# Kernel tuning notes

Measured on AMD Instinct MI355X. Metric: run time of the kernel, lower is better.

The kernel has to match this reference:

```python
import jax, jax.numpy as jnp
import numpy as np
from jax import lax

BN_EPS = 1e-5

@jax.custom_vjp
def ste_sign(x):
    # Binarize to {-1, +1} (sign; 0 maps to 0 like torch.sign, negligible measure)
    return jnp.sign(x)

def _ste_fwd(x):
    return jnp.sign(x), x

def _ste_bwd(x, g):
    # Straight-through estimator: pass gradient where |x| <= 1
    return (g * (jnp.abs(x) <= 1.0).astype(g.dtype),)

ste_sign.defvjp(_ste_fwd, _ste_bwd)

def bin_conv3x3(x, w, stride=1):
    # Binarize both activations and weights, then 3x3 conv, padding=1, no bias
    xb = ste_sign(x)
    wb = ste_sign(w)
    return lax.conv_general_dilated(
        xb, wb, window_strides=(stride, stride), padding=((1, 1), (1, 1)),
        dimension_numbers=('NCHW', 'OIHW', 'NCHW'))

def batchnorm_inf(x, gamma, beta, mean, var):
    # Inference-mode BatchNorm2d over channel dim (axis=1)
    scale = gamma * lax.rsqrt(var + BN_EPS)
    shift = beta - mean * scale
    return x * scale[None, :, None, None] + shift[None, :, None, None]

def hardtanh(x):
    # SelfTanh modeled as hardtanh (standard BNN activation with STE-style grad)
    return jnp.clip(x, -1.0, 1.0)

def setup_inputs() -> dict:
    key = jax.random.key(0)
    ks = jax.random.split(key, 3)
    N, C, H, W = 64, 256, 56, 56
    x = jax.random.normal(ks[0], (N, C, H, W), dtype=jnp.float32)
    w1 = jax.random.normal(ks[1], (C, C, 3, 3), dtype=jnp.float32) * (1.0 / math_sqrt(9 * C))
    w2 = jax.random.normal(ks[2], (C, C, 3, 3), dtype=jnp.float32) * (1.0 / math_sqrt(9 * C))
    ones = jnp.ones((C,), jnp.float32)
    zeros = jnp.zeros((C,), jnp.float32)
    return {
        'x': x,
        'w1': w1, 'g1': ones, 'b1': zeros, 'm1': zeros, 'v1': ones,
        'w2': w2, 'g2': ones, 'b2': zeros, 'm2': zeros, 'v2': ones,
    }

def math_sqrt(v):
    return float(np.sqrt(v))

def reference(x, w1, g1, b1, m1, v1, w2, g2, b2, m2, v2):
    residual = x
    out = bin_conv3x3(x, w1, stride=1)
    out = batchnorm_inf(out, g1, b1, m1, v1)
    out = hardtanh(out)
    out = bin_conv3x3(out, w2, stride=1)
    out = batchnorm_inf(out, g2, b2, m2, v2)
    out = out + residual
    out = hardtanh(out)
    return out
```

## Files before the change

### kernel.cpp

```cpp
#include <hip/hip_runtime.h>
#include <stdint.h>


#define NB 64
#define C  256
#define H  56
#define W  56
#define HP 58
#define PPIX 272
#define SLOT (HP * PPIX)
#define OST 272

typedef int v4i __attribute__((ext_vector_type(4)));

__global__ __launch_bounds__(256)
void pack_x_kernel(const float* __restrict__ x, int8_t* __restrict__ Aq) {
    const int h = blockIdx.x, n = blockIdx.y;
    const int w  = threadIdx.x & 63;
    const int cq = threadIdx.x >> 6;

    __shared__ int8_t st[56 * OST];

    const float* xp = x + (((size_t)n * C + cq * 64) * H + h) * W + w;
#pragma unroll
    for (int i = 0; i < 16; ++i) {
        uint32_t u = 0;
#pragma unroll
        for (int b = 0; b < 4; ++b) {
            float v = (w < 56) ? xp[(size_t)(i * 4 + b) * (H * W)] : 0.0f;
            uint32_t t = (v < 0.0f) ? 0xFFu : ((v != 0.0f) ? 1u : 0u);
            u |= t << (8 * b);
        }
        if (w < 56)
            *(uint32_t*)(st + w * OST + cq * 64 + i * 4) = u;
    }
    __syncthreads();
    int8_t* dst = Aq + (((size_t)n * HP + h + 1) * HP + 1) * C;
    for (int idx = threadIdx.x; idx < 56 * 16; idx += 256) {
        int pix = idx >> 4, c16 = idx & 15;
        *(v4i*)(dst + (size_t)pix * C + c16 * 16) =
            *(const v4i*)(st + pix * OST + c16 * 16);
    }
}

__global__ __launch_bounds__(64)
void pack_w_kernel(const float* __restrict__ wa, const float* __restrict__ wb,
                   int8_t* __restrict__ B1, int8_t* __restrict__ B2) {
    const int kstep = blockIdx.x;
    const int nfrag = blockIdx.y;
    const float* wsrc = blockIdx.z ? wb : wa;
    int8_t* dst       = blockIdx.z ? B2 : B1;
    const int lane = threadIdx.x, quad = lane >> 4, l16 = lane & 15;
    const int co = nfrag * 16 + l16;
    uint32_t pk[4];
#pragma unroll
    for (int d = 0; d < 4; ++d) {
        uint32_t u = 0;
#pragma unroll
        for (int bb = 0; bb < 4; ++bb) {
            int k = kstep * 64 + quad * 16 + d * 4 + bb;
            int tap = k >> 8, ci = k & 255;
            float v = wsrc[((size_t)co * C + ci) * 9 + tap];
            uint32_t t = (v < 0.0f) ? 0xFFu : ((v != 0.0f) ? 1u : 0u);
            u |= t << (8 * bb);
        }
        pk[d] = u;
    }
    uint4 st; st.x = pk[0]; st.y = pk[1]; st.z = pk[2]; st.w = pk[3];
    *(uint4*)(dst + ((size_t)(nfrag * 36 + kstep) * 64 + lane) * 16) = st;
}

__global__ __launch_bounds__(256)
void halo_zero_kernel(int8_t* __restrict__ Aq, int8_t* __restrict__ Bq) {
    const int n = blockIdx.x;
    int8_t* buf = blockIdx.y ? Bq : Aq;
    const v4i z = (v4i){0, 0, 0, 0};
    for (int idx = threadIdx.x; idx < 228 * 16; idx += 256) {
        int px = idx >> 4, c16 = idx & 15;
        int row, col;
        if (px < 58)       { row = 0;  col = px; }
        else if (px < 116) { row = 57; col = px - 58; }
        else { int i = px - 116; row = 1 + (i >> 1); col = (i & 1) * 57; }
        *(v4i*)(buf + (((size_t)n * HP + row) * HP + col) * C + c16 * 16) = z;
    }
}

__global__ __launch_bounds__(256)
void bn_prep_kernel(const float* g1, const float* b1, const float* m1, const float* v1,
                    const float* g2, const float* b2, const float* m2, const float* v2,
                    float* __restrict__ sc, float* __restrict__ sh) {
    const int co = threadIdx.x;
    const float* g = blockIdx.x ? g2 : g1;
    const float* b = blockIdx.x ? b2 : b1;
    const float* m = blockIdx.x ? m2 : m1;
    const float* v = blockIdx.x ? v2 : v1;
    double scd = (double)g[co] / sqrt((double)v[co] + 1e-5);
    sc[blockIdx.x * C + co] = (float)scd;
    sh[blockIdx.x * C + co] = (float)((double)b[co] - (double)m[co] * scd);
}

template <int STAGE>
__global__ __launch_bounds__(512, 4)
void mconv_kernel(const int8_t* __restrict__ Aq, const int8_t* __restrict__ Bpk,
                  const float* __restrict__ scp, const float* __restrict__ shp,
                  const float* __restrict__ resid,
                  int8_t* __restrict__ Bout, float* __restrict__ out) {
    const int h2 = blockIdx.x;
    const int n  = blockIdx.y;
    const int tid = threadIdx.x;
    const int wv = tid >> 6, lane = tid & 63, quad = lane >> 4, l16 = lane & 15;

    __shared__ int8_t lds[4 * SLOT];

    const int8_t* gA = Aq + ((size_t)n * HP + h2 * 2) * HP * C;
    for (int idx = tid; idx < 4 * HP * 16; idx += 512) {
        int pix = idx >> 4, c16 = idx & 15;
        *(v4i*)(lds + pix * PPIX + c16 * 16) =
            *(const v4i*)(gA + (size_t)pix * C + c16 * 16);
    }
    __syncthreads();

    int abase[7];
#pragma unroll
    for (int f = 0; f < 7; ++f) {
        int mm = f * 16 + l16;
        int hl = (mm >= 56) ? 1 : 0;
        int w  = mm - 56 * hl;
        abase[f] = hl * SLOT + w * PPIX + quad * 16;
    }

    const int8_t* bq[2];
#pragma unroll
    for (int nf = 0; nf < 2; ++nf)
        bq[nf] = Bpk + (size_t)((wv * 2 + nf) * 36) * 1024 + lane * 16;

    v4i bcur[2];
#pragma unroll
    for (int nf = 0; nf < 2; ++nf) bcur[nf] = *(const v4i*)(bq[nf]);

    v4i acc[7][2];
#pragma unroll
    for (int f = 0; f < 7; ++f)
#pragma unroll
        for (int nf = 0; nf < 2; ++nf) acc[f][nf] = (v4i){0, 0, 0, 0};

#pragma unroll 1
    for (int t = 0; t < 9; ++t) {
        const int r = (t >= 6) ? 2 : ((t >= 3) ? 1 : 0);
        const int c = t - 3 * r;
        const int au = r * SLOT + c * PPIX;
#pragma unroll
        for (int ci = 0; ci < 4; ++ci) {
            v4i bnxt[2];
#pragma unroll
            for (int nf = 0; nf < 2; ++nf)
                bnxt[nf] = *(const v4i*)(bq[nf] + (ci + 1) * 1024);
            v4i afr[7];
#pragma unroll
            for (int f = 0; f < 7; ++f)
                afr[f] = *(const v4i*)(lds + abase[f] + au + ci * 64);
            __builtin_amdgcn_s_setprio(1);
#pragma unroll
            for (int f = 0; f < 7; ++f)
#pragma unroll
                for (int nf = 0; nf < 2; ++nf)
                    acc[f][nf] = __builtin_amdgcn_mfma_i32_16x16x64_i8(
                        afr[f], bcur[nf], acc[f][nf], 0, 0, 0);
            __builtin_amdgcn_s_setprio(0);
#pragma unroll
            for (int nf = 0; nf < 2; ++nf) bcur[nf] = bnxt[nf];
        }
#pragma unroll
        for (int nf = 0; nf < 2; ++nf) bq[nf] += 4096;
    }

    if (STAGE == 1) {
        __syncthreads();
#pragma unroll
        for (int nf = 0; nf < 2; ++nf) {
            const int co = (wv * 2 + nf) * 16 + l16;
            const float scale = scp[co], shift = shp[co];
#pragma unroll
            for (int f = 0; f < 7; ++f) {
#pragma unroll
                for (int reg = 0; reg < 4; ++reg) {
                    int mm = f * 16 + quad * 4 + reg;
                    float v = __fadd_rn(__fmul_rn((float)acc[f][nf][reg], scale), shift);
                    int8_t t8 = (v < 0.0f) ? (int8_t)-1
                              : ((v != 0.0f) ? (int8_t)1 : (int8_t)0);
                    lds[mm * OST + co] = t8;
                }
            }
        }
        __syncthreads();
        for (int idx = tid; idx < 112 * 16; idx += 512) {
            int mm = idx >> 4, c16 = idx & 15;
            int hl = (mm >= 56) ? 1 : 0;
            int ww = mm - 56 * hl;
            int oh = h2 * 2 + hl;
            *(v4i*)(Bout + (((size_t)n * HP + oh + 1) * HP + ww + 1) * C + c16 * 16)
                = *(const v4i*)(lds + mm * OST + c16 * 16);
        }
    } else {
#pragma unroll
        for (int nf = 0; nf < 2; ++nf) {
            const int co = (wv * 2 + nf) * 16 + l16;
            const float scale = scp[co], shift = shp[co];
#pragma unroll
            for (int f = 0; f < 7; ++f) {
                int mmb = f * 16 + quad * 4;
                int hl = (mmb >= 56) ? 1 : 0;
                int w0 = mmb - 56 * hl;
                int oh = h2 * 2 + hl;
                size_t ridx = (((size_t)n * C + co) * H + oh) * W + w0;
                float4 rv = *(const float4*)(resid + ridx);
                float rr[4] = {rv.x, rv.y, rv.z, rv.w};
                float oo[4];
#pragma unroll
                for (int reg = 0; reg < 4; ++reg) {
                    float v = __fadd_rn(__fmul_rn((float)acc[f][nf][reg], scale), shift);
                    float o = v + rr[reg];
                    oo[reg] = fminf(1.0f, fmaxf(-1.0f, o));
                }
                float4 ov; ov.x = oo[0]; ov.y = oo[1]; ov.z = oo[2]; ov.w = oo[3];
                *(float4*)(out + ridx) = ov;
            }
        }
    }
}

extern "C" void kernel_launch(void* const* d_in, const int* in_sizes, int n_in,
                              void* d_out, int out_size, void* d_ws, size_t ws_size,
                              hipStream_t stream) {
    const float* x  = (const float*)d_in[0];
    const float* w1 = (const float*)d_in[1];
    const float* g1 = (const float*)d_in[2];
    const float* b1 = (const float*)d_in[3];
    const float* m1 = (const float*)d_in[4];
    const float* v1 = (const float*)d_in[5];
    const float* w2 = (const float*)d_in[6];
    const float* g2 = (const float*)d_in[7];
    const float* b2 = (const float*)d_in[8];
    const float* m2 = (const float*)d_in[9];
    const float* v2 = (const float*)d_in[10];
    float* out = (float*)d_out;

    uint8_t* ws = (uint8_t*)d_ws;
    const size_t ASZ = (size_t)NB * HP * HP * C;
    const size_t WPK = (size_t)16 * 36 * 64 * 16;
    int8_t* Aq   = (int8_t*)(ws);
    int8_t* Bq   = (int8_t*)(ws + ASZ);
    int8_t* Bpk1 = (int8_t*)(ws + 2 * ASZ);
    int8_t* Bpk2 = (int8_t*)(ws + 2 * ASZ + WPK);
    float*  scb  = (float*)(ws + 2 * ASZ + 2 * WPK);
    float*  shb  = (float*)(ws + 2 * ASZ + 2 * WPK + 2048);

    halo_zero_kernel<<<dim3(NB, 2), 256, 0, stream>>>(Aq, Bq);
    bn_prep_kernel<<<dim3(2), 256, 0, stream>>>(g1, b1, m1, v1, g2, b2, m2, v2,
                                                scb, shb);
    pack_w_kernel<<<dim3(36, 16, 2), 64, 0, stream>>>(w1, w2, Bpk1, Bpk2);
    pack_x_kernel<<<dim3(H, NB), 256, 0, stream>>>(x, Aq);
    mconv_kernel<1><<<dim3(28, NB), 512, 0, stream>>>(Aq, Bpk1, scb, shb,
                                                      nullptr, Bq, nullptr);
    mconv_kernel<2><<<dim3(28, NB), 512, 0, stream>>>(Bq, Bpk2, scb + C, shb + C,
                                                      x, nullptr, out);
}
```

Before: 605.6 us.

## Process one output row per block instead of two, raising occupancy

```diff
diff --git a/kernel.cpp b/kernel.cpp
--- a/kernel.cpp
+++ b/kernel.cpp
@@ -100,47 +100,37 @@
 }
 
 template <int STAGE>
-__global__ __launch_bounds__(512, 4)
+__global__ __launch_bounds__(512, 6)
 void mconv_kernel(const int8_t* __restrict__ Aq, const int8_t* __restrict__ Bpk,
                   const float* __restrict__ scp, const float* __restrict__ shp,
                   const float* __restrict__ resid,
                   int8_t* __restrict__ Bout, float* __restrict__ out) {
-    const int h2 = blockIdx.x;
+    const int oh = blockIdx.x;
     const int n  = blockIdx.y;
     const int tid = threadIdx.x;
     const int wv = tid >> 6, lane = tid & 63, quad = lane >> 4, l16 = lane & 15;
 
-    __shared__ int8_t lds[4 * SLOT];
-
-    const int8_t* gA = Aq + ((size_t)n * HP + h2 * 2) * HP * C;
-    for (int idx = tid; idx < 4 * HP * 16; idx += 512) {
+    __shared__ int8_t lds[3 * SLOT + 8 * PPIX];
+
+    const int8_t* gA = Aq + ((size_t)n * HP + oh) * HP * C;
+    for (int idx = tid; idx < 3 * HP * 16; idx += 512) {
         int pix = idx >> 4, c16 = idx & 15;
         *(v4i*)(lds + pix * PPIX + c16 * 16) =
             *(const v4i*)(gA + (size_t)pix * C + c16 * 16);
     }
     __syncthreads();
 
-    int abase[7];
-#pragma unroll
-    for (int f = 0; f < 7; ++f) {
-        int mm = f * 16 + l16;
-        int hl = (mm >= 56) ? 1 : 0;
-        int w  = mm - 56 * hl;
-        abase[f] = hl * SLOT + w * PPIX + quad * 16;
-    }
-
-    const int8_t* bq[2];
-#pragma unroll
-    for (int nf = 0; nf < 2; ++nf)
-        bq[nf] = Bpk + (size_t)((wv * 2 + nf) * 36) * 1024 + lane * 16;
-
-    v4i bcur[2];
-#pragma unroll
-    for (int nf = 0; nf < 2; ++nf) bcur[nf] = *(const v4i*)(bq[nf]);
-
-    v4i acc[7][2];
-#pragma unroll
-    for (int f = 0; f < 7; ++f)
+    int abase[4];
+#pragma unroll
+    for (int f = 0; f < 4; ++f)
+        abase[f] = (f * 16 + l16) * PPIX + quad * 16;
+
+    const int8_t* bq0 = Bpk + (size_t)((wv * 2 + 0) * 36) * 1024 + lane * 16;
+    const int8_t* bq1 = Bpk + (size_t)((wv * 2 + 1) * 36) * 1024 + lane * 16;
+
+    v4i acc[4][2];
+#pragma unroll
+    for (int f = 0; f < 4; ++f)
 #pragma unroll
         for (int nf = 0; nf < 2; ++nf) acc[f][nf] = (v4i){0, 0, 0, 0};
 
@@ -151,27 +141,24 @@
         const int au = r * SLOT + c * PPIX;
 #pragma unroll
         for (int ci = 0; ci < 4; ++ci) {
-            v4i bnxt[2];
-#pragma unroll
-            for (int nf = 0; nf < 2; ++nf)
-                bnxt[nf] = *(const v4i*)(bq[nf] + (ci + 1) * 1024);
-            v4i afr[7];
-#pragma unroll
-            for (int f = 0; f < 7; ++f)
+            v4i b0 = *(const v4i*)(bq0 + ci * 1024);
+            v4i b1 = *(const v4i*)(bq1 + ci * 1024);
+            v4i afr[4];
+#pragma unroll
+            for (int f = 0; f < 4; ++f)
                 afr[f] = *(const v4i*)(lds + abase[f] + au + ci * 64);
             __builtin_amdgcn_s_setprio(1);
 #pragma unroll
-            for (int f = 0; f < 7; ++f)
-#pragma unroll
-                for (int nf = 0; nf < 2; ++nf)
-                    acc[f][nf] = __builtin_amdgcn_mfma_i32_16x16x64_i8(
-                        afr[f], bcur[nf], acc[f][nf], 0, 0, 0);
+            for (int f = 0; f < 4; ++f) {
+                acc[f][0] = __builtin_amdgcn_mfma_i32_16x16x64_i8(
+                    afr[f], b0, acc[f][0], 0, 0, 0);
+                acc[f][1] = __builtin_amdgcn_mfma_i32_16x16x64_i8(
+                    afr[f], b1, acc[f][1], 0, 0, 0);
+            }
             __builtin_amdgcn_s_setprio(0);
-#pragma unroll
-            for (int nf = 0; nf < 2; ++nf) bcur[nf] = bnxt[nf];
-        }
-#pragma unroll
-        for (int nf = 0; nf < 2; ++nf) bq[nf] += 4096;
+        }
+        bq0 += 4096;
+        bq1 += 4096;
     }
 
     if (STAGE == 1) {
@@ -181,25 +168,24 @@
             const int co = (wv * 2 + nf) * 16 + l16;
             const float scale = scp[co], shift = shp[co];
 #pragma unroll
-            for (int f = 0; f < 7; ++f) {
+            for (int f = 0; f < 4; ++f) {
 #pragma unroll
                 for (int reg = 0; reg < 4; ++reg) {
                     int mm = f * 16 + quad * 4 + reg;
-                    float v = __fadd_rn(__fmul_rn((float)acc[f][nf][reg], scale), shift);
-                    int8_t t8 = (v < 0.0f) ? (int8_t)-1
-                              : ((v != 0.0f) ? (int8_t)1 : (int8_t)0);
-                    lds[mm * OST + co] = t8;
+                    if (mm < 56) {
+                        float v = __fadd_rn(__fmul_rn((float)acc[f][nf][reg], scale), shift);
+                        int8_t t8 = (v < 0.0f) ? (int8_t)-1
+                                  : ((v != 0.0f) ? (int8_t)1 : (int8_t)0);
+                        lds[mm * OST + co] = t8;
+                    }
                 }
             }
         }
         __syncthreads();
-        for (int idx = tid; idx < 112 * 16; idx += 512) {
-            int mm = idx >> 4, c16 = idx & 15;
-            int hl = (mm >= 56) ? 1 : 0;
-            int ww = mm - 56 * hl;
-            int oh = h2 * 2 + hl;
+        for (int idx = tid; idx < 56 * 16; idx += 512) {
+            int ww = idx >> 4, c16 = idx & 15;
             *(v4i*)(Bout + (((size_t)n * HP + oh + 1) * HP + ww + 1) * C + c16 * 16)
-                = *(const v4i*)(lds + mm * OST + c16 * 16);
+                = *(const v4i*)(lds + ww * OST + c16 * 16);
         }
     } else {
 #pragma unroll
@@ -207,23 +193,22 @@
             const int co = (wv * 2 + nf) * 16 + l16;
             const float scale = scp[co], shift = shp[co];
 #pragma unroll
-            for (int f = 0; f < 7; ++f) {
+            for (int f = 0; f < 4; ++f) {
                 int mmb = f * 16 + quad * 4;
-                int hl = (mmb >= 56) ? 1 : 0;
-                int w0 = mmb - 56 * hl;
-                int oh = h2 * 2 + hl;
-                size_t ridx = (((size_t)n * C + co) * H + oh) * W + w0;
-                float4 rv = *(const float4*)(resid + ridx);
-                float rr[4] = {rv.x, rv.y, rv.z, rv.w};
-                float oo[4];
-#pragma unroll
-                for (int reg = 0; reg < 4; ++reg) {
-                    float v = __fadd_rn(__fmul_rn((float)acc[f][nf][reg], scale), shift);
-                    float o = v + rr[reg];
-                    oo[reg] = fminf(1.0f, fmaxf(-1.0f, o));
+                if (mmb < 56) {
+                    size_t ridx = (((size_t)n * C + co) * H + oh) * W + mmb;
+                    float4 rv = *(const float4*)(resid + ridx);
+                    float rr[4] = {rv.x, rv.y, rv.z, rv.w};
+                    float oo[4];
+#pragma unroll
+                    for (int reg = 0; reg < 4; ++reg) {
+                        float v = __fadd_rn(__fmul_rn((float)acc[f][nf][reg], scale), shift);
+                        float o = v + rr[reg];
+                        oo[reg] = fminf(1.0f, fmaxf(-1.0f, o));
+                    }
+                    float4 ov; ov.x = oo[0]; ov.y = oo[1]; ov.z = oo[2]; ov.w = oo[3];
+                    *(float4*)(out + ridx) = ov;
                 }
-                float4 ov; ov.x = oo[0]; ov.y = oo[1]; ov.z = oo[2]; ov.w = oo[3];
-                *(float4*)(out + ridx) = ov;
             }
         }
     }
@@ -260,8 +245,8 @@
                                                 scb, shb);
     pack_w_kernel<<<dim3(36, 16, 2), 64, 0, stream>>>(w1, w2, Bpk1, Bpk2);
     pack_x_kernel<<<dim3(H, NB), 256, 0, stream>>>(x, Aq);
-    mconv_kernel<1><<<dim3(28, NB), 512, 0, stream>>>(Aq, Bpk1, scb, shb,
-                                                      nullptr, Bq, nullptr);
-    mconv_kernel<2><<<dim3(28, NB), 512, 0, stream>>>(Bq, Bpk2, scb + C, shb + C,
-                                                      x, nullptr, out);
-}
+    mconv_kernel<1><<<dim3(H, NB), 512, 0, stream>>>(Aq, Bpk1, scb, shb,
+                                                     nullptr, Bq, nullptr);
+    mconv_kernel<2><<<dim3(H, NB), 512, 0, stream>>>(Bq, Bpk2, scb + C, shb + C,
+                                                     x, nullptr, out);
+}
```

After: 690.6 us. 1.14x slower.
